# Kernel tuning notes

Measured on AMD Instinct MI355X. Metric: run time of the kernel, lower is better.

## Reference

```python
import jax, jax.numpy as jnp
import numpy as np

# NTU spatial neighbor triples (1-indexed joint labels in the original repo; we
# subtract 1 to get valid 0-based indices into the J=25 joint axis).
_NTU = np.array([[17,1,13],[21,2,1],[4,3,21],[3,4,3],[21,5,6],[5,6,7],[6,7,8],
                 [7,8,7],[10,9,23],[11,10,9],[12,11,10],[25,12,11],[1,13,14],
                 [13,14,15],[14,15,16],[15,16,15],[18,17,1],[19,18,17],
                 [20,19,18],[19,20,19],[9,21,5],[23,22,23],[8,23,22],
                 [25,24,25],[24,25,12]], dtype=np.int32) - 1

B, C, J, T, CO = 64, 3, 25, 256, 64
SIG_C = 4 + 16 + 64  # (C+1) + (C+1)^2 + (C+1)^3 with time augmentation, depth 3
EPS = 1e-5


def _exp_levels(d):
    # truncated tensor exponential of a linear increment, depth 3
    d2 = jnp.einsum('ni,nj->nij', d, d)
    d3 = jnp.einsum('nij,nk->nijk', d2, d)
    return d, d2 * 0.5, d3 / 6.0


def _sig3(path):
    # path: (N, 3, c). Signature with basepoint=0 via Chen's relation, depth 3.
    incs = jnp.concatenate([path[:, :1, :], path[:, 1:, :] - path[:, :-1, :]], axis=1)
    S1, S2, S3 = _exp_levels(incs[:, 0])
    for t in range(1, incs.shape[1]):  # fixed small stream length (3)
        B1, B2, B3 = _exp_levels(incs[:, t])
        S3 = S3 + B3 + jnp.einsum('ni,njk->nijk', S1, B2) + jnp.einsum('nij,nk->nijk', S2, B1)
        S2 = S2 + B2 + jnp.einsum('ni,nj->nij', S1, B1)
        S1 = S1 + B1
    N = path.shape[0]
    return jnp.concatenate([S1, S2.reshape(N, -1), S3.reshape(N, -1)], axis=1)


def _signet(inp, W, b):
    # inp: (N, 3, C) -> augment with time in [0,1] (signatory.Augment include_time)
    N = inp.shape[0]
    time = jnp.broadcast_to(jnp.linspace(0.0, 1.0, 3, dtype=inp.dtype)[None, :, None], (N, 3, 1))
    aug = jnp.concatenate([time, inp], axis=-1)  # (N, 3, C+1)
    return _sig3(aug) @ W + b


def _bn(x, g, b):
    # training-mode BatchNorm2d (biased variance) over (B, H, W) per channel
    m = x.mean(axis=(0, 2, 3), keepdims=True)
    v = x.var(axis=(0, 2, 3), keepdims=True)
    return (x - m) * jax.lax.rsqrt(v + EPS) * g.reshape(1, -1, 1, 1) + b.reshape(1, -1, 1, 1)


def setup_inputs() -> dict:
    key = jax.random.key(0)
    ks = jax.random.split(key, 12)
    inp = {
        'x': jax.random.normal(ks[0], (B, C, J, T), jnp.float32),
        'conv_w': jax.random.normal(ks[1], (CO, C, 1, 3), jnp.float32) * 0.3,
        'conv_b': jax.random.normal(ks[2], (CO,), jnp.float32) * 0.05,
        'raw_gamma': jnp.ones((CO,), jnp.float32),
        'raw_beta': jnp.zeros((CO,), jnp.float32),
        'sp_W': jax.random.normal(ks[3], (SIG_C, CO), jnp.float32) * 0.1,
        'sp_b': jax.random.normal(ks[4], (CO,), jnp.float32) * 0.05,
        'tp_W': jax.random.normal(ks[5], (SIG_C, CO), jnp.float32) * 0.1,
        'tp_b': jax.random.normal(ks[6], (CO,), jnp.float32) * 0.05,
        'ps_w': jax.random.normal(ks[7], (CO, 2 * CO), jnp.float32) * 0.1,
        'ps_b': jax.random.normal(ks[8], (CO,), jnp.float32) * 0.05,
        'ps_gamma': jnp.ones((CO,), jnp.float32),
        'ps_beta': jnp.zeros((CO,), jnp.float32),
        'fu_w': jax.random.normal(ks[9], (CO, 2 * CO), jnp.float32) * 0.1,
        'fu_b': jax.random.normal(ks[10], (CO,), jnp.float32) * 0.05,
        'fu_gamma': jnp.ones((CO,), jnp.float32),
        'fu_beta': jnp.zeros((CO,), jnp.float32),
        'neighbors': jnp.asarray(_NTU, jnp.int32),
    }
    return inp


def reference(x, conv_w, conv_b, raw_gamma, raw_beta, sp_W, sp_b, tp_W, tp_b,
              ps_w, ps_b, ps_gamma, ps_beta, fu_w, fu_b, fu_gamma, fu_beta,
              neighbors):
    Bx, Cx, Jx, Tx = x.shape
    # --- raw branch: Conv2d (1,3) pad (0,1) -> ReLU -> BN ---
    x_conv = jax.lax.conv_general_dilated(
        x, conv_w, window_strides=(1, 1), padding=((0, 0), (1, 1)),
        dimension_numbers=('NCHW', 'OIHW', 'NCHW')) + conv_b.reshape(1, -1, 1, 1)
    x_conv = _bn(jax.nn.relu(x_conv), raw_gamma, raw_beta)

    # --- spatial paths: gather neighbor triples per joint ---
    # x[:, :, neighbors, :]: (B, C, J, 3, T) -> (J, B, T, 3, C)
    sp = jnp.transpose(x[:, :, neighbors, :], (2, 0, 4, 3, 1)).reshape(Jx * Bx * Tx, 3, Cx)
    spatial_sig = _signet(sp, sp_W, sp_b)  # (J*B*T, CO)
    spatial_sig = jnp.transpose(spatial_sig.reshape(Jx, Bx, Tx, CO), (1, 3, 0, 2))  # (B,CO,J,T)

    # --- temporal paths: sliding window of 3 with replicate padding ---
    x_ps = jnp.pad(x, ((0, 0), (0, 0), (0, 0), (1, 1)), mode='edge')  # (B,C,J,T+2)
    win = jnp.arange(Tx)[:, None] + jnp.arange(3)[None, :]  # (T, 3)
    xw = x_ps[:, :, :, win]  # (B, C, J, T, 3)
    tp = jnp.transpose(xw, (3, 0, 2, 4, 1)).reshape(Tx * Bx * Jx, 3, Cx)
    temporal_sig = _signet(tp, tp_W, tp_b)  # (T*B*J, CO)
    temporal_sig = jnp.transpose(temporal_sig.reshape(Tx, Bx, Jx, CO), (1, 3, 2, 0))  # (B,CO,J,T)

    # --- ps_fusion: 1x1 conv -> ReLU -> BN ---
    sig = jnp.concatenate([spatial_sig, temporal_sig], axis=1)  # (B, 2CO, J, T)
    sig = jnp.einsum('bihw,oi->bohw', sig, ps_w) + ps_b.reshape(1, -1, 1, 1)
    sig = _bn(jax.nn.relu(sig), ps_gamma, ps_beta)

    # --- final fusion with conv branch ---
    x_out = jnp.concatenate([x_conv, sig], axis=1)  # (B, 2CO, J, T)
    x_out = jnp.einsum('bihw,oi->bohw', x_out, fu_w) + fu_b.reshape(1, -1, 1, 1)
    x_out = _bn(jax.nn.relu(x_out), fu_gamma, fu_beta)
    return x_out
```

## Files before the change

kernel.cpp:

```cpp
#include <hip/hip_runtime.h>
#include <hip/hip_bf16.h>
#include <stdint.h>

#define B_   64
#define C_   3
#define J_   25
#define T_   256
#define CO_  64
#define N_   (B_*J_*T_)
#define SIGD 84
#define FSTR 177
#define WST  136

typedef short   s16x8  __attribute__((ext_vector_type(8)));
typedef __bf16  bf16x8 __attribute__((ext_vector_type(8)));
typedef float   f32x4  __attribute__((ext_vector_type(4)));
typedef float   f32x2  __attribute__((ext_vector_type(2)));

__device__ __forceinline__ unsigned short f2b(float f) {
    unsigned int u = __float_as_uint(f);
    u += 0x7fffu + ((u >> 16) & 1u);
    return (unsigned short)(u >> 16);
}
__device__ __forceinline__ float b2f(unsigned int bits_lo16) {
    return __uint_as_float(bits_lo16 << 16);
}
__device__ __forceinline__ unsigned int pack2(float a, float b) {
    return (unsigned int)f2b(a) | ((unsigned int)f2b(b) << 16);
}
__device__ __forceinline__ void split2(float f, unsigned short& h, unsigned short& l) {
    h = f2b(f);
    l = f2b(f - b2f((unsigned int)h));
}

__device__ __forceinline__ void sig3(const float v0[4], const float v1[4],
                                     const float v2[4], float* __restrict__ S) {
    float* S1 = S;
    float* S2 = S + 4;
    float* S3 = S + 20;
    #pragma unroll
    for (int i = 0; i < 4; i++) S1[i] = v0[i];
    #pragma unroll
    for (int i = 0; i < 4; i++)
        #pragma unroll
        for (int j = 0; j < 4; j++) S2[i*4+j] = 0.5f * v0[i] * v0[j];
    #pragma unroll
    for (int i = 0; i < 4; i++)
        #pragma unroll
        for (int j = 0; j < 4; j++)
            #pragma unroll
            for (int k = 0; k < 4; k++)
                S3[i*16+j*4+k] = S2[i*4+j] * v0[k] * (1.f/3.f);

    #pragma unroll
    for (int s = 0; s < 2; s++) {
        const float* v = (s == 0) ? v1 : v2;
        float B2[16], v3[4];
        #pragma unroll
        for (int k = 0; k < 4; k++) v3[k] = v[k] * (1.f/3.f);
        #pragma unroll
        for (int i = 0; i < 4; i++)
            #pragma unroll
            for (int j = 0; j < 4; j++) B2[i*4+j] = 0.5f * v[i] * v[j];
        #pragma unroll
        for (int i = 0; i < 4; i++)
            #pragma unroll
            for (int j = 0; j < 4; j++)
                #pragma unroll
                for (int k = 0; k < 4; k++)
                    S3[i*16+j*4+k] += B2[i*4+j]*v3[k] + S1[i]*B2[j*4+k] + S2[i*4+j]*v[k];
        #pragma unroll
        for (int i = 0; i < 4; i++)
            #pragma unroll
            for (int j = 0; j < 4; j++) S2[i*4+j] += B2[i*4+j] + S1[i]*v[j];
        #pragma unroll
        for (int i = 0; i < 4; i++) S1[i] += v[i];
    }
}

__global__ void k_prep(const float* __restrict__ sp_W, const float* __restrict__ sp_b,
                       const float* __restrict__ tp_W, const float* __restrict__ tp_b,
                       const float* __restrict__ ps_w, const float* __restrict__ ps_b,
                       float* __restrict__ wsig_t, float* __restrict__ cb) {
    int k = blockIdx.x;
    int o = threadIdx.x;
    if (k < SIGD) {
        float v = 0.f;
        for (int i = 0; i < 64; i++) v += sp_W[k*64+i] * ps_w[o*128+i];
        wsig_t[k*64 + o] = v;
    } else if (k < 2*SIGD) {
        int m = k - SIGD;
        float v = 0.f;
        for (int i = 0; i < 64; i++) v += tp_W[m*64+i] * ps_w[o*128+64+i];
        wsig_t[k*64 + o] = v;
    } else {
        float a = ps_b[o];
        for (int i = 0; i < 64; i++)
            a += ps_w[o*128+i]*sp_b[i] + ps_w[o*128+64+i]*tp_b[i];
        cb[o] = a;
    }
}

__global__ __launch_bounds__(256) void k_sig(const float* __restrict__ x,
                                             const int* __restrict__ nbr,
                                             const float* __restrict__ wsig_t,
                                             const float* __restrict__ cb,
                                             const float* __restrict__ conv_w,
                                             const float* __restrict__ conv_b,
                                             unsigned short* __restrict__ zcat) {
    __shared__ float feats[64*FSTR];

    const int i       = threadIdx.x;
    const int quarter = blockIdx.x & 3;
    const int bj      = blockIdx.x >> 2;
    const int b       = bj / J_, j = bj % J_;
    const int loc_base = bj*T_ + quarter*64;

    if (i < 128) {
        const int lt   = i >> 1;
        const int path = i & 1;
        const int t    = quarter*64 + lt;
        float p0[4], p1[4], p2[4];
        p0[0] = 0.f; p1[0] = 0.5f; p2[0] = 1.0f;
        if (path == 0) {
            int n0 = nbr[j*3+0], n1 = nbr[j*3+1], n2 = nbr[j*3+2];
            #pragma unroll
            for (int c = 0; c < 3; c++) {
                const float* xc = x + ((size_t)(b*3+c)*J_)*T_ + t;
                p0[c+1] = xc[n0*T_];
                p1[c+1] = xc[n1*T_];
                p2[c+1] = xc[n2*T_];
            }
        } else {
            int tm = (t > 0)    ? t-1 : 0;
            int tp = (t < T_-1) ? t+1 : T_-1;
            #pragma unroll
            for (int c = 0; c < 3; c++) {
                const float* xr = x + ((size_t)(b*3+c)*J_ + j)*T_;
                p0[c+1] = xr[tm];
                p1[c+1] = xr[t];
                p2[c+1] = xr[tp];
            }
        }
        float v0[4], v1[4], v2[4];
        #pragma unroll
        for (int d = 0; d < 4; d++) { v0[d]=p0[d]; v1[d]=p1[d]-p0[d]; v2[d]=p2[d]-p1[d]; }
        float S[SIGD];
        sig3(v0, v1, v2, S);
        float* frow = feats + lt*FSTR + path*SIGD;
        #pragma unroll
        for (int m = 0; m < SIGD; m++) frow[m] = S[m];
    } else {
        const int ci  = i - 128;
        const int lt  = ci >> 1;
        const int chh = ci & 1;
        const int t   = quarter*64 + lt;
        const int loc = loc_base + lt;
        float xm[3], x0[3], xp[3];
        #pragma unroll
        for (int c = 0; c < 3; c++) {
            const float* xr = x + ((size_t)(b*3+c)*J_ + j)*T_;
            xm[c] = (t > 0)     ? xr[t-1] : 0.f;
            x0[c] = xr[t];
            xp[c] = (t < T_-1)  ? xr[t+1] : 0.f;
        }
        unsigned int packed[16];
        #pragma unroll
        for (int oo2 = 0; oo2 < 16; oo2++) {
            float r[2];
            #pragma unroll
            for (int e = 0; e < 2; e++) {
                int o = chh*32 + oo2*2 + e;
                float acc = conv_b[o];
                #pragma unroll
                for (int c = 0; c < 3; c++) {
                    const float* wr = conv_w + (o*3+c)*3;
                    acc += wr[0]*xm[c] + wr[1]*x0[c] + wr[2]*xp[c];
                }
                r[e] = fmaxf(acc, 0.f);
            }
            packed[oo2] = pack2(r[0], r[1]);
        }
        uint4* dst = (uint4*)(zcat + (size_t)loc*128 + chh*32);
        #pragma unroll
        for (int k = 0; k < 4; k++)
            dst[k] = make_uint4(packed[k*4+0], packed[k*4+1], packed[k*4+2], packed[k*4+3]);
    }
    __syncthreads();

    const int og = __builtin_amdgcn_readfirstlane(i >> 6);
    const int lt = i & 63;
    const int loc = loc_base + lt;
    const float* wt = wsig_t + og*16;
    f32x2 acc2[8];
    {
        const f32x2* cbp = (const f32x2*)(cb + og*16);
        #pragma unroll
        for (int p = 0; p < 8; p++) acc2[p] = cbp[p];
    }
    const float* frow = feats + lt*FSTR;
    #pragma unroll 4
    for (int k = 0; k < 2*SIGD; k++) {
        float f = frow[k];
        f32x2 f2 = { f, f };
        const f32x2* w2 = (const f32x2*)(wt + k*64);
        #pragma unroll
        for (int p = 0; p < 8; p++) acc2[p] += f2 * w2[p];
    }
    unsigned int pk[8];
    #pragma unroll
    for (int p = 0; p < 8; p++)
        pk[p] = pack2(fmaxf(acc2[p][0],0.f), fmaxf(acc2[p][1],0.f));
    uint4* dst = (uint4*)(zcat + (size_t)loc*128 + 64 + og*16);
    dst[0] = make_uint4(pk[0], pk[1], pk[2], pk[3]);
    dst[1] = make_uint4(pk[4], pk[5], pk[6], pk[7]);
}

template<int NCH>
__global__ __launch_bounds__(256) void k_stats(const unsigned short* __restrict__ z,
                                               float* __restrict__ sum,
                                               float* __restrict__ ssq) {
    constexpr int G  = NCH/8;
    constexpr int LP = 256/G;
    const int i = threadIdx.x;
    const int g = i % G;
    const int lr = i / G;
    const int base = blockIdx.x * 1600;
    float s[8], qq[8];
    #pragma unroll
    for (int k = 0; k < 8; k++) { s[k] = 0.f; qq[k] = 0.f; }
    for (int l = lr; l < 1600; l += LP) {
        const uint4 v = *(const uint4*)(z + (size_t)(base + l)*NCH + g*8);
        unsigned int u[4] = { v.x, v.y, v.z, v.w };
        #pragma unroll
        for (int k = 0; k < 4; k++) {
            float f0 = b2f(u[k] & 0xffffu);
            float f1 = __uint_as_float(u[k] & 0xffff0000u);
            s[2*k]   += f0;  qq[2*k]   += f0*f0;
            s[2*k+1] += f1;  qq[2*k+1] += f1*f1;
        }
    }
    const int lane = i & 63, wv = i >> 6;
    for (int off = 32; off >= G; off >>= 1) {
        #pragma unroll
        for (int k = 0; k < 8; k++) {
            s[k]  += __shfl_down(s[k],  off);
            qq[k] += __shfl_down(qq[k], off);
        }
    }
    __shared__ float red[4][G][16];
    if (lane < G) {
        #pragma unroll
        for (int k = 0; k < 8; k++) { red[wv][lane][k] = s[k]; red[wv][lane][8+k] = qq[k]; }
    }
    __syncthreads();
    if (i < G*16) {
        int g2 = i >> 4, slot = i & 15;
        float v = red[0][g2][slot] + red[1][g2][slot] + red[2][g2][slot] + red[3][g2][slot];
        int ch = g2*8 + (slot & 7);
        atomicAdd((slot < 8 ? sum : ssq) + ch, v);
    }
}

__global__ void k_fin1(const float* __restrict__ sum_cp, const float* __restrict__ ssq_cp,
                       const float* __restrict__ raw_g, const float* __restrict__ raw_b,
                       const float* __restrict__ ps_g,  const float* __restrict__ ps_bt,
                       const float* __restrict__ fu_w,  const float* __restrict__ fu_b,
                       unsigned short* __restrict__ w12h, unsigned short* __restrict__ w12l,
                       float* __restrict__ w12s_t, float* __restrict__ fb2) {
    __shared__ float a[128], d[128];
    int i = threadIdx.x;
    const float inv = 1.f / (float)N_;
    {
        float m = sum_cp[i]*inv, v = ssq_cp[i]*inv - m*m;
        float sc = rsqrtf(v + 1e-5f) * raw_g[i];
        a[i] = sc; d[i] = raw_b[i] - m*sc;
    }
    {
        float m = sum_cp[64+i]*inv, v = ssq_cp[64+i]*inv - m*m;
        float sc = rsqrtf(v + 1e-5f) * ps_g[i];
        a[64+i] = sc; d[64+i] = ps_bt[i] - m*sc;
    }
    __syncthreads();
    int o = i;
    float fb = fu_b[o];
    for (int k = 0; k < 128; k++) {
        float w = fu_w[o*128 + k];
        fb += w * d[k];
        float ws = w * a[k];
        w12s_t[k*64 + o] = ws;
        unsigned short h, l;
        split2(ws, h, l);
        w12h[o*WST + k] = h;
        w12l[o*WST + k] = l;
    }
    for (int k = 128; k < WST; k++) { w12h[o*WST + k] = 0; w12l[o*WST + k] = 0; }
    fb2[o] = fb;
}

__global__ __launch_bounds__(256) void k_fu(const unsigned short* __restrict__ zcat,
                                            const unsigned short* __restrict__ w12h,
                                            const unsigned short* __restrict__ w12l,
                                            const float* __restrict__ w12s_t,
                                            const float* __restrict__ fb2,
                                            unsigned short* __restrict__ z_fu) {
    __shared__ __align__(16) unsigned short zt[128*WST];
    const int i = threadIdx.x;
    const int loc_base = blockIdx.x * 128;

    for (int c = i; c < 2048; c += 256) {
        int row = c >> 4, k = c & 15;
        s16x8 v = *(const s16x8*)(zcat + (size_t)(loc_base + row)*128 + k*8);
        *(s16x8*)(zt + row*WST + k*8) = v;
    }
    __syncthreads();

    const int lane = i & 63, wv = i >> 6;
    const int mrow = lane & 15, q = lane >> 4;
    const f32x4 zero = {0.f, 0.f, 0.f, 0.f};

    bf16x8 ap, bp;
    #pragma unroll
    for (int jj = 0; jj < 8; jj++) { ap[jj] = (__bf16)(float)mrow; bp[jj] = (__bf16)1.0f; }
    f32x4 pv = __builtin_amdgcn_mfma_f32_16x16x32_bf16(ap, bp, zero, 0, 0, 0);
    bool cC = true, cT = true;
    #pragma unroll
    for (int r = 0; r < 4; r++) {
        cC = cC && (pv[r] == 32.f*(float)(q*4 + r));
        cT = cT && (pv[r] == 32.f*(float)mrow);
    }
    const bool okC = (__ballot(cC) == ~0ull);
    const bool okT = (!okC) && (__ballot(cT) == ~0ull);

    if (okC || okT) {
        bf16x8 ah[4], al[4];
        {
            const unsigned short* arh = w12h + (size_t)(wv*16 + mrow)*WST + q*8;
            const unsigned short* arl = w12l + (size_t)(wv*16 + mrow)*WST + q*8;
            #pragma unroll
            for (int s = 0; s < 4; s++) {
                ah[s] = __builtin_bit_cast(bf16x8, *(const s16x8*)(arh + s*32));
                al[s] = __builtin_bit_cast(bf16x8, *(const s16x8*)(arl + s*32));
            }
        }
        f32x4 accs[8];
        #pragma unroll
        for (int lt8 = 0; lt8 < 8; lt8++) {
            const unsigned short* brow = zt + (size_t)(lt8*16 + mrow)*WST + q*8;
            f32x4 acc = zero;
            #pragma unroll
            for (int s = 0; s < 4; s++) {
                bf16x8 bfrag = __builtin_bit_cast(bf16x8, *(const s16x8*)(brow + s*32));
                acc = __builtin_amdgcn_mfma_f32_16x16x32_bf16(ah[s], bfrag, acc, 0, 0, 0);
                acc = __builtin_amdgcn_mfma_f32_16x16x32_bf16(al[s], bfrag, acc, 0, 0, 0);
            }
            accs[lt8] = acc;
        }
        __syncthreads();

        unsigned short* ot = zt;
        if (okC) {
            const float4 fbv = *(const float4*)(fb2 + wv*16 + q*4);
            #pragma unroll
            for (int lt8 = 0; lt8 < 8; lt8++) {
                int row = lt8*16 + mrow;
                int o   = wv*16 + q*4;
                uint2 w;
                w.x = pack2(fmaxf(accs[lt8][0]+fbv.x,0.f), fmaxf(accs[lt8][1]+fbv.y,0.f));
                w.y = pack2(fmaxf(accs[lt8][2]+fbv.z,0.f), fmaxf(accs[lt8][3]+fbv.w,0.f));
                *(uint2*)(ot + row*72 + o) = w;
            }
        } else {
            const float fb1 = fb2[wv*16 + mrow];
            #pragma unroll
            for (int lt8 = 0; lt8 < 8; lt8++) {
                #pragma unroll
                for (int r = 0; r < 4; r++) {
                    int row = lt8*16 + q*4 + r;
                    ot[row*72 + wv*16 + mrow] = f2b(fmaxf(accs[lt8][r]+fb1, 0.f));
                }
            }
        }
        __syncthreads();
        for (int c = i; c < 1024; c += 256) {
            int row = c >> 3, k = c & 7;
            s16x8 v = *(const s16x8*)(ot + row*72 + k*8);
            *(s16x8*)(z_fu + (size_t)(loc_base + row)*64 + k*8) = v;
        }
    } else {
        if (i < 128) {
            const unsigned short* fr = zt + i*WST;
            const int loc = loc_base + i;
            for (int og8 = 0; og8 < 8; og8++) {
                float acc[8];
                #pragma unroll
                for (int p = 0; p < 8; p++) acc[p] = fb2[og8*8 + p];
                for (int k = 0; k < 128; k++) {
                    float f = b2f(fr[k]);
                    const float* w = w12s_t + k*64 + og8*8;
                    #pragma unroll
                    for (int p = 0; p < 8; p++) acc[p] = fmaf(f, w[p], acc[p]);
                }
                #pragma unroll
                for (int p = 0; p < 8; p++)
                    z_fu[(size_t)loc*64 + og8*8 + p] = f2b(fmaxf(acc[p], 0.f));
            }
        }
    }
}

__global__ void k_fin2(const float* __restrict__ sum_f, const float* __restrict__ ssq_f,
                       const float* __restrict__ fu_g,
                       float* __restrict__ mf, float* __restrict__ rfg) {
    int o = threadIdx.x;
    const float inv = 1.f / (float)N_;
    float m = sum_f[o]*inv, v = ssq_f[o]*inv - m*m;
    mf[o] = m;
    rfg[o] = rsqrtf(v + 1e-5f) * fu_g[o];
}

__global__ __launch_bounds__(256) void k_out(const unsigned short* __restrict__ z_fu,
                                             const float* __restrict__ mf,
                                             const float* __restrict__ rfg,
                                             const float* __restrict__ fu_beta,
                                             float* __restrict__ out) {
    __shared__ __align__(16) unsigned short zt[256*66];
    const int i = threadIdx.x;
    const int bj = blockIdx.x;
    const int b = bj / J_, j = bj % J_;
    const int loc_base = bj * T_;

    for (int c = i; c < 2048; c += 256) {
        int row = c >> 3, k = c & 7;
        uint4 v = *(const uint4*)(z_fu + (size_t)(loc_base + row)*64 + k*8);
        unsigned int* dst = (unsigned int*)(zt + row*66 + k*8);
        dst[0] = v.x; dst[1] = v.y; dst[2] = v.z; dst[3] = v.w;
    }
    __syncthreads();

    const int t = i;
    const unsigned int* zrow = (const unsigned int*)zt + t*33;
    for (int o = 0; o < 64; o += 2) {
        unsigned int v = zrow[o >> 1];
        float f0 = b2f(v & 0xffffu);
        float f1 = __uint_as_float(v & 0xffff0000u);
        out[(((size_t)b*64 + o  )*J_ + j)*T_ + t] = (f0 - mf[o  ])*rfg[o  ] + fu_beta[o  ];
        out[(((size_t)b*64 + o+1)*J_ + j)*T_ + t] = (f1 - mf[o+1])*rfg[o+1] + fu_beta[o+1];
    }
}

extern "C" void kernel_launch(void* const* d_in, const int* in_sizes, int n_in,
                              void* d_out, int out_size, void* d_ws, size_t ws_size,
                              hipStream_t stream) {
    const float* x         = (const float*)d_in[0];
    const float* conv_w    = (const float*)d_in[1];
    const float* conv_b    = (const float*)d_in[2];
    const float* raw_gamma = (const float*)d_in[3];
    const float* raw_beta  = (const float*)d_in[4];
    const float* sp_W      = (const float*)d_in[5];
    const float* sp_b      = (const float*)d_in[6];
    const float* tp_W      = (const float*)d_in[7];
    const float* tp_b      = (const float*)d_in[8];
    const float* ps_w      = (const float*)d_in[9];
    const float* ps_b      = (const float*)d_in[10];
    const float* ps_gamma  = (const float*)d_in[11];
    const float* ps_beta   = (const float*)d_in[12];
    const float* fu_w      = (const float*)d_in[13];
    const float* fu_b      = (const float*)d_in[14];
    const float* fu_gamma  = (const float*)d_in[15];
    const float* fu_beta   = (const float*)d_in[16];
    const int*   neighbors = (const int*)d_in[17];

    char* ws = (char*)d_ws;
    unsigned short* zcat   = (unsigned short*)ws;
    unsigned short* z_fu   = (unsigned short*)(ws + 104857600);
    size_t off = 157286400;
    float* wsig_t = (float*)(ws + off);          off += 168*64*4;
    float* w12s_t = (float*)(ws + off);          off += 128*64*4;
    unsigned short* w12h = (unsigned short*)(ws + off); off += 64*WST*2;
    unsigned short* w12l = (unsigned short*)(ws + off); off += 64*WST*2;
    float* f32s   = (float*)(ws + off);
    float* cb     = f32s;
    float* fb2    = f32s + 64;
    float* mf     = f32s + 128;
    float* rfg    = f32s + 192;
    float* sum_cp = f32s + 256;
    float* ssq_cp = f32s + 384;
    float* sum_f  = f32s + 512;
    float* ssq_f  = f32s + 576;

    hipMemsetAsync(sum_cp, 0, 384*sizeof(float), stream);

    k_prep<<<169, 64, 0, stream>>>(sp_W, sp_b, tp_W, tp_b, ps_w, ps_b, wsig_t, cb);
    k_sig<<<6400, 256, 0, stream>>>(x, neighbors, wsig_t, cb, conv_w, conv_b, zcat);
    k_stats<128><<<256, 256, 0, stream>>>(zcat, sum_cp, ssq_cp);
    k_fin1<<<1, 64, 0, stream>>>(sum_cp, ssq_cp, raw_gamma, raw_beta,
                                 ps_gamma, ps_beta, fu_w, fu_b,
                                 w12h, w12l, w12s_t, fb2);
    k_fu<<<3200, 256, 0, stream>>>(zcat, w12h, w12l, w12s_t, fb2, z_fu);
    k_stats<64><<<256, 256, 0, stream>>>(z_fu, sum_f, ssq_f);
    k_fin2<<<1, 64, 0, stream>>>(sum_f, ssq_f, fu_gamma, mf, rfg);
    k_out<<<1600, 256, 0, stream>>>(z_fu, mf, rfg, fu_beta, (float*)d_out);
}
```

Measured before the change: 436.4 us.

## Fuse BatchNorm statistic reductions into producer kernels with slotted atomics

Removes the two standalone k_stats launches. k_sig and k_fu now compute per-channel sum and sum-of-squares on the tile they just wrote, reading it back right after a block barrier. The partial sums go into 8 slotted global accumulators, and k_fin1 and k_fin2 add the slots together. This avoids a second full pass over the large zcat and z_fu buffers. In exchange it issues many more global atomics, which can contend, and it relies on the block's own global writes being visible after __syncthreads.

```diff
diff --git a/kernel.cpp b/kernel.cpp
--- a/kernel.cpp
+++ b/kernel.cpp
@@ -107,7 +107,9 @@
                                              const float* __restrict__ cb,
                                              const float* __restrict__ conv_w,
                                              const float* __restrict__ conv_b,
-                                             unsigned short* __restrict__ zcat) {
+                                             unsigned short* __restrict__ zcat,
+                                             float* __restrict__ sum_cp8,
+                                             float* __restrict__ ssq_cp8) {
     __shared__ float feats[64*FSTR];
 
     const int i       = threadIdx.x;
@@ -188,81 +190,78 @@
     }
     __syncthreads();
 
-    const int og = __builtin_amdgcn_readfirstlane(i >> 6);
-    const int lt = i & 63;
-    const int loc = loc_base + lt;
-    const float* wt = wsig_t + og*16;
-    f32x2 acc2[8];
     {
-        const f32x2* cbp = (const f32x2*)(cb + og*16);
-        #pragma unroll
-        for (int p = 0; p < 8; p++) acc2[p] = cbp[p];
-    }
-    const float* frow = feats + lt*FSTR;
-    #pragma unroll 4
-    for (int k = 0; k < 2*SIGD; k++) {
-        float f = frow[k];
-        f32x2 f2 = { f, f };
-        const f32x2* w2 = (const f32x2*)(wt + k*64);
-        #pragma unroll
-        for (int p = 0; p < 8; p++) acc2[p] += f2 * w2[p];
-    }
-    unsigned int pk[8];
-    #pragma unroll
-    for (int p = 0; p < 8; p++)
-        pk[p] = pack2(fmaxf(acc2[p][0],0.f), fmaxf(acc2[p][1],0.f));
-    uint4* dst = (uint4*)(zcat + (size_t)loc*128 + 64 + og*16);
-    dst[0] = make_uint4(pk[0], pk[1], pk[2], pk[3]);
-    dst[1] = make_uint4(pk[4], pk[5], pk[6], pk[7]);
-}
-
-template<int NCH>
-__global__ __launch_bounds__(256) void k_stats(const unsigned short* __restrict__ z,
-                                               float* __restrict__ sum,
-                                               float* __restrict__ ssq) {
-    constexpr int G  = NCH/8;
-    constexpr int LP = 256/G;
-    const int i = threadIdx.x;
-    const int g = i % G;
-    const int lr = i / G;
-    const int base = blockIdx.x * 1600;
-    float s[8], qq[8];
-    #pragma unroll
-    for (int k = 0; k < 8; k++) { s[k] = 0.f; qq[k] = 0.f; }
-    for (int l = lr; l < 1600; l += LP) {
-        const uint4 v = *(const uint4*)(z + (size_t)(base + l)*NCH + g*8);
-        unsigned int u[4] = { v.x, v.y, v.z, v.w };
-        #pragma unroll
-        for (int k = 0; k < 4; k++) {
-            float f0 = b2f(u[k] & 0xffffu);
-            float f1 = __uint_as_float(u[k] & 0xffff0000u);
-            s[2*k]   += f0;  qq[2*k]   += f0*f0;
-            s[2*k+1] += f1;  qq[2*k+1] += f1*f1;
-        }
-    }
-    const int lane = i & 63, wv = i >> 6;
-    for (int off = 32; off >= G; off >>= 1) {
-        #pragma unroll
-        for (int k = 0; k < 8; k++) {
-            s[k]  += __shfl_down(s[k],  off);
-            qq[k] += __shfl_down(qq[k], off);
-        }
-    }
-    __shared__ float red[4][G][16];
-    if (lane < G) {
-        #pragma unroll
-        for (int k = 0; k < 8; k++) { red[wv][lane][k] = s[k]; red[wv][lane][8+k] = qq[k]; }
-    }
+        const int og = __builtin_amdgcn_readfirstlane(i >> 6);
+        const int lt = i & 63;
+        const int loc = loc_base + lt;
+        const float* wt = wsig_t + og*16;
+        f32x2 acc2[8];
+        {
+            const f32x2* cbp = (const f32x2*)(cb + og*16);
+            #pragma unroll
+            for (int p = 0; p < 8; p++) acc2[p] = cbp[p];
+        }
+        const float* frow = feats + lt*FSTR;
+        #pragma unroll 4
+        for (int k = 0; k < 2*SIGD; k++) {
+            float f = frow[k];
+            f32x2 f2 = { f, f };
+            const f32x2* w2 = (const f32x2*)(wt + k*64);
+            #pragma unroll
+            for (int p = 0; p < 8; p++) acc2[p] += f2 * w2[p];
+        }
+        unsigned int pk[8];
+        #pragma unroll
+        for (int p = 0; p < 8; p++)
+            pk[p] = pack2(fmaxf(acc2[p][0],0.f), fmaxf(acc2[p][1],0.f));
+        uint4* dst = (uint4*)(zcat + (size_t)loc*128 + 64 + og*16);
+        dst[0] = make_uint4(pk[0], pk[1], pk[2], pk[3]);
+        dst[1] = make_uint4(pk[4], pk[5], pk[6], pk[7]);
+    }
+
     __syncthreads();
-    if (i < G*16) {
-        int g2 = i >> 4, slot = i & 15;
-        float v = red[0][g2][slot] + red[1][g2][slot] + red[2][g2][slot] + red[3][g2][slot];
-        int ch = g2*8 + (slot & 7);
-        atomicAdd((slot < 8 ? sum : ssq) + ch, v);
-    }
-}
-
-__global__ void k_fin1(const float* __restrict__ sum_cp, const float* __restrict__ ssq_cp,
+    {
+        const int g2  = i & 15;
+        const int lr2 = i >> 4;
+        float s[8], q[8];
+        #pragma unroll
+        for (int k = 0; k < 8; k++) { s[k] = 0.f; q[k] = 0.f; }
+        #pragma unroll
+        for (int li = 0; li < 4; li++) {
+            const int l = lr2 + li*16;
+            const uint4 v = *(const uint4*)(zcat + (size_t)(loc_base + l)*128 + g2*8);
+            unsigned int u[4] = { v.x, v.y, v.z, v.w };
+            #pragma unroll
+            for (int k = 0; k < 4; k++) {
+                float f0 = b2f(u[k] & 0xffffu);
+                float f1 = __uint_as_float(u[k] & 0xffff0000u);
+                s[2*k]   += f0;  q[2*k]   += f0*f0;
+                s[2*k+1] += f1;  q[2*k+1] += f1*f1;
+            }
+        }
+        #pragma unroll
+        for (int off = 16; off <= 32; off <<= 1) {
+            #pragma unroll
+            for (int k = 0; k < 8; k++) {
+                s[k] += __shfl_xor(s[k], off);
+                q[k] += __shfl_xor(q[k], off);
+            }
+        }
+        const int lane = i & 63;
+        if (lane < 16) {
+            const int slot = blockIdx.x & 7;
+            float* sb = sum_cp8 + slot*128 + g2*8;
+            float* qb = ssq_cp8 + slot*128 + g2*8;
+            #pragma unroll
+            for (int k = 0; k < 8; k++) {
+                atomicAdd(sb + k, s[k]);
+                atomicAdd(qb + k, q[k]);
+            }
+        }
+    }
+}
+
+__global__ void k_fin1(const float* __restrict__ sum_cp8, const float* __restrict__ ssq_cp8,
                        const float* __restrict__ raw_g, const float* __restrict__ raw_b,
                        const float* __restrict__ ps_g,  const float* __restrict__ ps_bt,
                        const float* __restrict__ fu_w,  const float* __restrict__ fu_b,
@@ -271,13 +270,18 @@
     __shared__ float a[128], d[128];
     int i = threadIdx.x;
     const float inv = 1.f / (float)N_;
+    float s0 = 0.f, q0 = 0.f, s1 = 0.f, q1 = 0.f;
+    for (int sl = 0; sl < 8; sl++) {
+        s0 += sum_cp8[sl*128 + i];       q0 += ssq_cp8[sl*128 + i];
+        s1 += sum_cp8[sl*128 + 64 + i];  q1 += ssq_cp8[sl*128 + 64 + i];
+    }
     {
-        float m = sum_cp[i]*inv, v = ssq_cp[i]*inv - m*m;
+        float m = s0*inv, v = q0*inv - m*m;
         float sc = rsqrtf(v + 1e-5f) * raw_g[i];
         a[i] = sc; d[i] = raw_b[i] - m*sc;
     }
     {
-        float m = sum_cp[64+i]*inv, v = ssq_cp[64+i]*inv - m*m;
+        float m = s1*inv, v = q1*inv - m*m;
         float sc = rsqrtf(v + 1e-5f) * ps_g[i];
         a[64+i] = sc; d[64+i] = ps_bt[i] - m*sc;
     }
@@ -303,7 +307,9 @@
                                             const unsigned short* __restrict__ w12l,
                                             const float* __restrict__ w12s_t,
                                             const float* __restrict__ fb2,
-                                            unsigned short* __restrict__ z_fu) {
+                                            unsigned short* __restrict__ z_fu,
+                                            float* __restrict__ sum_f8,
+                                            float* __restrict__ ssq_f8) {
     __shared__ __align__(16) unsigned short zt[128*WST];
     const int i = threadIdx.x;
     const int loc_base = blockIdx.x * 128;
@@ -407,14 +413,56 @@
             }
         }
     }
-}
-
-__global__ void k_fin2(const float* __restrict__ sum_f, const float* __restrict__ ssq_f,
+
+    __syncthreads();
+    {
+        const int g3  = i & 7;
+        const int lr3 = i >> 3;
+        float s[8], q2[8];
+        #pragma unroll
+        for (int k = 0; k < 8; k++) { s[k] = 0.f; q2[k] = 0.f; }
+        #pragma unroll
+        for (int li = 0; li < 4; li++) {
+            const int l = lr3 + li*32;
+            const uint4 v = *(const uint4*)(z_fu + (size_t)(loc_base + l)*64 + g3*8);
+            unsigned int u[4] = { v.x, v.y, v.z, v.w };
+            #pragma unroll
+            for (int k = 0; k < 4; k++) {
+                float f0 = b2f(u[k] & 0xffffu);
+                float f1 = __uint_as_float(u[k] & 0xffff0000u);
+                s[2*k]   += f0;  q2[2*k]   += f0*f0;
+                s[2*k+1] += f1;  q2[2*k+1] += f1*f1;
+            }
+        }
+        #pragma unroll
+        for (int off = 8; off <= 32; off <<= 1) {
+            #pragma unroll
+            for (int k = 0; k < 8; k++) {
+                s[k]  += __shfl_xor(s[k],  off);
+                q2[k] += __shfl_xor(q2[k], off);
+            }
+        }
+        if (lane < 8) {
+            const int slot = blockIdx.x & 7;
+            float* sb = sum_f8 + slot*64 + g3*8;
+            float* qb = ssq_f8 + slot*64 + g3*8;
+            #pragma unroll
+            for (int k = 0; k < 8; k++) {
+                atomicAdd(sb + k, s[k]);
+                atomicAdd(qb + k, q2[k]);
+            }
+        }
+    }
+}
+
+__global__ void k_fin2(const float* __restrict__ sum_f8, const float* __restrict__ ssq_f8,
                        const float* __restrict__ fu_g,
                        float* __restrict__ mf, float* __restrict__ rfg) {
     int o = threadIdx.x;
     const float inv = 1.f / (float)N_;
-    float m = sum_f[o]*inv, v = ssq_f[o]*inv - m*m;
+    float sm = 0.f, sq = 0.f;
+    for (int sl = 0; sl < 8; sl++) { sm += sum_f8[sl*64 + o]; sq += ssq_f8[sl*64 + o]; }
+    float m = sm*inv, v = sq*inv - m*m;
     mf[o] = m;
     rfg[o] = rsqrtf(v + 1e-5f) * fu_g[o];
 }
@@ -480,25 +528,25 @@
     unsigned short* w12h = (unsigned short*)(ws + off); off += 64*WST*2;
     unsigned short* w12l = (unsigned short*)(ws + off); off += 64*WST*2;
     float* f32s   = (float*)(ws + off);
-    float* cb     = f32s;
-    float* fb2    = f32s + 64;
-    float* mf     = f32s + 128;
-    float* rfg    = f32s + 192;
-    float* sum_cp = f32s + 256;
-    float* ssq_cp = f32s + 384;
-    float* sum_f  = f32s + 512;
-    float* ssq_f  = f32s + 576;
-
-    hipMemsetAsync(sum_cp, 0, 384*sizeof(float), stream);
+    float* cb      = f32s;
+    float* fb2     = f32s + 64;
+    float* mf      = f32s + 128;
+    float* rfg     = f32s + 192;
+    float* sum_cp8 = f32s + 256;
+    float* ssq_cp8 = f32s + 1280;
+    float* sum_f8  = f32s + 2304;
+    float* ssq_f8  = f32s + 2816;
+
+    hipMemsetAsync(sum_cp8, 0, 3072*sizeof(float), stream);
 
     k_prep<<<169, 64, 0, stream>>>(sp_W, sp_b, tp_W, tp_b, ps_w, ps_b, wsig_t, cb);
-    k_sig<<<6400, 256, 0, stream>>>(x, neighbors, wsig_t, cb, conv_w, conv_b, zcat);
-    k_stats<128><<<256, 256, 0, stream>>>(zcat, sum_cp, ssq_cp);
-    k_fin1<<<1, 64, 0, stream>>>(sum_cp, ssq_cp, raw_gamma, raw_beta,
+    k_sig<<<6400, 256, 0, stream>>>(x, neighbors, wsig_t, cb, conv_w, conv_b, zcat,
+                                    sum_cp8, ssq_cp8);
+    k_fin1<<<1, 64, 0, stream>>>(sum_cp8, ssq_cp8, raw_gamma, raw_beta,
                                  ps_gamma, ps_beta, fu_w, fu_b,
                                  w12h, w12l, w12s_t, fb2);
-    k_fu<<<3200, 256, 0, stream>>>(zcat, w12h, w12l, w12s_t, fb2, z_fu);
-    k_stats<64><<<256, 256, 0, stream>>>(z_fu, sum_f, ssq_f);
-    k_fin2<<<1, 64, 0, stream>>>(sum_f, ssq_f, fu_gamma, mf, rfg);
+    k_fu<<<3200, 256, 0, stream>>>(zcat, w12h, w12l, w12s_t, fb2, z_fu,
+                                   sum_f8, ssq_f8);
+    k_fin2<<<1, 64, 0, stream>>>(sum_f8, ssq_f8, fu_gamma, mf, rfg);
     k_out<<<1600, 256, 0, stream>>>(z_fu, mf, rfg, fu_beta, (float*)d_out);
 }
```

Result: slower. 1.158 ms (+165.4%).

## Fuse fusion-layer BatchNorm statistics into k_fu epilogue with slotted atomics

Applied to the files above, without the earlier changes.

Removes the separate k_stats<64> pass over z_fu by having each k_fu block re-read its just-written 128 rows and reduce per-channel sum and sum-of-squares. The partial sums are combined with shuffles and shared memory, then atomically added into one of 32 slot arrays to limit atomic contention. k_fin2 now sums the slots. This saves a full re-read of z_fu and one kernel launch, at the cost of an extra syncthreads, a per-block epilogue that reloads its own output from global memory, and atomics whose ordering can vary between runs.

```diff
diff --git a/kernel.cpp b/kernel.cpp
--- a/kernel.cpp
+++ b/kernel.cpp
@@ -11,6 +11,7 @@
 #define SIGD 84
 #define FSTR 177
 #define WST  136
+#define NSLOT 32
 
 typedef short   s16x8  __attribute__((ext_vector_type(8)));
 typedef __bf16  bf16x8 __attribute__((ext_vector_type(8)));
@@ -303,7 +304,9 @@
                                             const unsigned short* __restrict__ w12l,
                                             const float* __restrict__ w12s_t,
                                             const float* __restrict__ fb2,
-                                            unsigned short* __restrict__ z_fu) {
+                                            unsigned short* __restrict__ z_fu,
+                                            float* __restrict__ sum_f,
+                                            float* __restrict__ ssq_f) {
     __shared__ __align__(16) unsigned short zt[128*WST];
     const int i = threadIdx.x;
     const int loc_base = blockIdx.x * 128;
@@ -407,6 +410,54 @@
             }
         }
     }
+
+    __syncthreads();
+    {
+        const int g3  = i & 7;
+        const int lr3 = i >> 3;
+        float s[8], q2[8];
+        #pragma unroll
+        for (int k = 0; k < 8; k++) { s[k] = 0.f; q2[k] = 0.f; }
+        #pragma unroll
+        for (int li = 0; li < 4; li++) {
+            const int l = lr3 + li*32;
+            const uint4 v = *(const uint4*)(z_fu + (size_t)(loc_base + l)*64 + g3*8);
+            unsigned int u[4] = { v.x, v.y, v.z, v.w };
+            #pragma unroll
+            for (int k = 0; k < 4; k++) {
+                float f0 = b2f(u[k] & 0xffffu);
+                float f1 = __uint_as_float(u[k] & 0xffff0000u);
+                s[2*k]   += f0;  q2[2*k]   += f0*f0;
+                s[2*k+1] += f1;  q2[2*k+1] += f1*f1;
+            }
+        }
+        #pragma unroll
+        for (int off = 8; off <= 32; off <<= 1) {
+            #pragma unroll
+            for (int k = 0; k < 8; k++) {
+                s[k]  += __shfl_xor(s[k],  off);
+                q2[k] += __shfl_xor(q2[k], off);
+            }
+        }
+        float* red = (float*)zt;
+        if (lane < 8) {
+            #pragma unroll
+            for (int k = 0; k < 8; k++) {
+                red[(wv*8 + g3)*16 + k]     = s[k];
+                red[(wv*8 + g3)*16 + 8 + k] = q2[k];
+            }
+        }
+        __syncthreads();
+        if (i < 128) {
+            const int ch = i >> 1, which = i & 1;
+            const int g = ch >> 3, k = ch & 7;
+            const int idx = which*8 + k;
+            float t0 = red[(0*8+g)*16 + idx] + red[(1*8+g)*16 + idx]
+                     + red[(2*8+g)*16 + idx] + red[(3*8+g)*16 + idx];
+            const int slot = blockIdx.x & (NSLOT-1);
+            atomicAdd((which ? ssq_f : sum_f) + slot*64 + ch, t0);
+        }
+    }
 }
 
 __global__ void k_fin2(const float* __restrict__ sum_f, const float* __restrict__ ssq_f,
@@ -414,7 +465,9 @@
                        float* __restrict__ mf, float* __restrict__ rfg) {
     int o = threadIdx.x;
     const float inv = 1.f / (float)N_;
-    float m = sum_f[o]*inv, v = ssq_f[o]*inv - m*m;
+    float sm = 0.f, sq = 0.f;
+    for (int sl = 0; sl < NSLOT; sl++) { sm += sum_f[sl*64 + o]; sq += ssq_f[sl*64 + o]; }
+    float m = sm*inv, v = sq*inv - m*m;
     mf[o] = m;
     rfg[o] = rsqrtf(v + 1e-5f) * fu_g[o];
 }
@@ -487,9 +540,9 @@
     float* sum_cp = f32s + 256;
     float* ssq_cp = f32s + 384;
     float* sum_f  = f32s + 512;
-    float* ssq_f  = f32s + 576;
-
-    hipMemsetAsync(sum_cp, 0, 384*sizeof(float), stream);
+    float* ssq_f  = sum_f + NSLOT*64;
+
+    hipMemsetAsync(sum_cp, 0, (size_t)(256 + NSLOT*128)*sizeof(float), stream);
 
     k_prep<<<169, 64, 0, stream>>>(sp_W, sp_b, tp_W, tp_b, ps_w, ps_b, wsig_t, cb);
     k_sig<<<6400, 256, 0, stream>>>(x, neighbors, wsig_t, cb, conv_w, conv_b, zcat);
@@ -497,8 +550,8 @@
     k_fin1<<<1, 64, 0, stream>>>(sum_cp, ssq_cp, raw_gamma, raw_beta,
                                  ps_gamma, ps_beta, fu_w, fu_b,
                                  w12h, w12l, w12s_t, fb2);
-    k_fu<<<3200, 256, 0, stream>>>(zcat, w12h, w12l, w12s_t, fb2, z_fu);
-    k_stats<64><<<256, 256, 0, stream>>>(z_fu, sum_f, ssq_f);
+    k_fu<<<3200, 256, 0, stream>>>(zcat, w12h, w12l, w12s_t, fb2, z_fu,
+                                   sum_f, ssq_f);
     k_fin2<<<1, 64, 0, stream>>>(sum_f, ssq_f, fu_gamma, mf, rfg);
     k_out<<<1600, 256, 0, stream>>>(z_fu, mf, rfg, fu_beta, (float*)d_out);
 }
```

Measured after the change: 413.7 us. 1.05x faster.
